# Performance work log

Measured on AMD Instinct MI355X. Metric: run time of the kernel, lower is better.

The kernel has to match this reference:

```python
import jax, jax.numpy as jnp
import numpy as np
from jax import lax

DN = ('NCHW', 'OIHW', 'NCHW')

def conv(x, k):
    return lax.conv_general_dilated(x, k, (1, 1), 'SAME', dimension_numbers=DN)

def conv_adj(y, k):
    # adjoint of SAME stride-1 conv: correlate with spatially-flipped, channel-transposed kernel
    return conv(y, jnp.flip(k, (2, 3)).transpose(1, 0, 2, 3))

def setup_inputs() -> dict:
    key = jax.random.key(0)
    ks = jax.random.split(key, 8)
    B, H, W = 8, 512, 512
    Cw, Ch = 4, 32
    return {
        'sino': jax.random.normal(ks[0], (B, 1, H, W), jnp.float32),
        'x': jax.random.normal(ks[1], (B, 1, H, W), jnp.float32),
        'laam': jnp.asarray([0.05], jnp.float32),
        'miu': jnp.asarray([0.01], jnp.float32),
        'Kw': jax.random.normal(ks[2], (Cw, 1, 3, 3), jnp.float32) * 0.1,
        'Ka': jax.random.normal(ks[3], (1, 1, 5, 5), jnp.float32) * 0.1,
        'W1': jax.random.normal(ks[4], (Ch, 1, 3, 3), jnp.float32) * 0.05,
        'b1': jnp.zeros((Ch,), jnp.float32),
        'W2': jax.random.normal(ks[5], (Ch, Ch, 3, 3), jnp.float32) * 0.05,
        'b2': jnp.zeros((Ch,), jnp.float32),
        'W3': jax.random.normal(ks[6], (1, Ch, 3, 3), jnp.float32) * 0.05,
        'b3': jnp.zeros((1,), jnp.float32),
    }

def reference(sino, x, laam, miu, Kw, Ka, W1, b1, W2, b2, W3, b3):
    mu = miu  # shape (1,), broadcasts as scalar

    def Wop(u):  return conv(u, Kw)          # analysis transform, [B,Cw,H,W]
    def WTop(v): return conv_adj(v, Kw)      # synthesis (adjoint)
    def Aop(u):  return conv(u, Ka)          # system operator surrogate
    def ATop(s): return conv_adj(s, Ka)

    def cnn(u):
        h = jax.nn.relu(conv(u, W1) + b1[None, :, None, None])
        h = jax.nn.relu(conv(h, W2) + b2[None, :, None, None])
        return u + conv(h, W3) + b3[None, :, None, None]

    def AWx(p):  # (A^T A + mu W^T W) p
        return ATop(Aop(p)) + mu * WTop(Wop(p))

    # --- MetaInvH forward ---
    Wu = Wop(x)
    dnz = jax.nn.relu(Wu - laam) - jax.nn.relu(-Wu - laam)  # soft threshold
    rhs = ATop(sino) + WTop(dnz) * miu
    uk0 = cnn(x)
    res = AWx(uk0) - rhs

    # --- CG_alg, 5 iterations + final half step ---
    xk, r, p = uk0, res, -res
    for _ in range(5):
        Ap = Aop(p)                                   # [B,1,H,W]
        Wp = Wop(p)                                   # [B,Cw,H,W]
        pATAp = jnp.sum(Ap * Ap, axis=(1, 2, 3))      # [B]
        pWTWp = mu * jnp.sum(Wp * Wp, axis=(1, 2, 3)) # [B]
        rTr = jnp.sum(r * r, axis=(1, 2, 3))
        al = (rTr / (pWTWp + pATAp))[:, None, None, None]
        xk = xk + al * p
        r = r + al * (ATop(Ap) + mu * WTop(Wp))
        be = (jnp.sum(r * r, axis=(1, 2, 3)) / rTr)[:, None, None, None]
        p = -r + be * p
    Ap = Aop(p)
    Wp = Wop(p)
    pATAp = jnp.sum(Ap * Ap, axis=(1, 2, 3))
    pWTWp = mu * jnp.sum(Wp * Wp, axis=(1, 2, 3))
    rTr = jnp.sum(r * r, axis=(1, 2, 3))
    al = (rTr / (pWTWp + pATAp))[:, None, None, None]
    return xk + al * p
```

## Files before the change

kernel.cpp:

```cpp
#include <hip/hip_runtime.h>

#define HH 512
#define WW 512
#define BB 8
#define IMG (HH*WW)
#define NTOT (BB*IMG)

typedef float f32x4 __attribute__((ext_vector_type(4)));
typedef _Float16 half8 __attribute__((ext_vector_type(8)));

__device__ inline uint f2h2(float a, float b) {
  uint d; asm("v_cvt_pkrtz_f16_f32 %0, %1, %2" : "=v"(d) : "v"(a), "v"(b)); return d;
}
__device__ inline uint pkfma(uint a, uint b, uint c) {
  uint d; asm("v_pk_fma_f16 %0, %1, %2, %3" : "=v"(d) : "v"(a), "v"(b), "v"(c)); return d;
}
__device__ inline uint pkmax0(uint a) {
  uint d, z = 0u; asm("v_pk_max_f16 %0, %1, %2" : "=v"(d) : "v"(a), "v"(z)); return d;
}

__device__ inline void atomic_block_sum(float part, float* red, float* dst) {
  for (int off = 32; off > 0; off >>= 1) part += __shfl_down(part, off, 64);
  int lane = threadIdx.x & 63, w = threadIdx.x >> 6;
  if (lane == 0) red[w] = part;
  __syncthreads();
  if (threadIdx.x == 0) atomicAdd(dst, red[0] + red[1] + red[2] + red[3]);
}

__global__ void k_prep(const float* __restrict__ Ka, const float* __restrict__ Kw,
                       const float* __restrict__ miu,
                       const float* __restrict__ W1, const float* __restrict__ b1,
                       const float* __restrict__ W2, const float* __restrict__ W3,
                       float* __restrict__ G, ushort* __restrict__ w2pk,
                       uint* __restrict__ w1pk, uint* __restrict__ b1pk,
                       ushort* __restrict__ w3fr, float* __restrict__ scal) {
  __shared__ float lka[25], lkw[36], lw1[288], lw3[288];
  int tid = threadIdx.x;
  if (tid < 192) scal[tid] = 0.f;
  if (tid < 25) lka[tid] = Ka[tid];
  if (tid < 36) lkw[tid] = Kw[tid];
  if (tid < 256) { lw1[tid] = W1[tid]; lw3[tid] = W3[tid]; }
  if (tid < 32) { lw1[256+tid] = W1[256+tid]; lw3[256+tid] = W3[256+tid]; }
  __syncthreads();
  if (tid < 81) {
    int oy = tid / 9 - 4, ox = tid % 9 - 4;
    float mu = miu[0];
    float ga = 0.f;
    for (int dy = 0; dy < 5; dy++)
      for (int dx = 0; dx < 5; dx++) {
        int ey = dy + oy, ex = dx + ox;
        if (ey >= 0 && ey < 5 && ex >= 0 && ex < 5) ga += lka[dy*5+dx] * lka[ey*5+ex];
      }
    float gw = 0.f;
    if (oy >= -2 && oy <= 2 && ox >= -2 && ox <= 2) {
      for (int ch = 0; ch < 4; ch++)
        for (int dy = 0; dy < 3; dy++)
          for (int dx = 0; dx < 3; dx++) {
            int ey = dy + oy, ex = dx + ox;
            if (ey >= 0 && ey < 3 && ex >= 0 && ex < 3)
              gw += lkw[ch*9 + dy*3+dx] * lkw[ch*9 + ey*3+ex];
          }
    }
    G[tid] = ga + mu * gw;
  }
  #pragma unroll 1
  for (int k = 0; k < 36; k++) {
    int i = tid + k*256;
    int j = i & 7, l = (i >> 3) & 63, f = i >> 9;
    int t5 = f >> 1, h = f & 1;
    int co = 16*h + (l & 15), ci = 8*(l >> 4) + j;
    w2pk[i] = (ushort)(f2h2(W2[(co*32 + ci)*9 + t5], 0.f) & 0xffffu);
  }
  if (tid < 144) {
    int cp = tid / 9, t = tid % 9;
    w1pk[tid] = f2h2(lw1[(2*cp)*9 + t], lw1[(2*cp+1)*9 + t]);
  }
  if (tid < 16) b1pk[tid] = f2h2(b1[2*tid], b1[2*tid+1]);
  for (int k = 0; k < 2; k++) {
    int i = tid + k*256;
    int j = i & 7, l = i >> 3;
    int tap = l & 15, ch = 8*(l >> 4) + j;
    w3fr[i] = (tap < 9) ? (ushort)(f2h2(lw3[ch*9 + tap], 0.f) & 0xffffu) : (ushort)0;
  }
}

__launch_bounds__(512)
__global__ void k_cnn(const float* __restrict__ x,
                      const ushort* __restrict__ w2pk, const uint* __restrict__ w1pk,
                      const uint* __restrict__ b1pk, const ushort* __restrict__ w3fr,
                      const float* __restrict__ b2, const float* __restrict__ b3,
                      float* __restrict__ xk) {
  __shared__ __align__(16) uint  xs_h2[528];
  __shared__ __align__(16) uint  h1u[7040];
  __shared__ __align__(16) uint  h2u[5472];

  const int tid = threadIdx.x;
  const int bimg = blockIdx.z;
  const int oy0 = blockIdx.y * 16, ox0 = blockIdx.x * 16;
  const float* xim = x + (size_t)bimg * IMG;

  for (int i = tid; i < 528; i += 512) {
    int ly = i / 24, lx = i % 24;
    int gy = oy0 + ly - 3, gx = ox0 + lx - 4;
    float v = 0.f;
    if ((unsigned)gy < HH && (unsigned)gx < WW) v = xim[gy*WW + gx];
    xs_h2[i] = f2h2(v, v);
  }
  __syncthreads();

  {
    const int cp = tid & 15;
    const int sg = tid >> 4;
    uint w1r[9];
    #pragma unroll
    for (int k = 0; k < 9; k++) w1r[k] = w1pk[cp*9 + k];
    const uint b1v = b1pk[cp];
    const int kg = cp >> 2, cl = cp & 3;
    #pragma unroll 1
    for (int s = sg; s < 100; s += 32) {
      int row = s / 5, st = s - 5*row;
      int px0 = st * 4;
      uint acc0 = b1v, acc1 = b1v, acc2 = b1v, acc3 = b1v;
      #pragma unroll
      for (int ky = 0; ky < 3; ky++) {
        int base = (row + ky) * 24 + px0;
        uint4 xa = *(const uint4*)&xs_h2[base];
        uint4 xb = *(const uint4*)&xs_h2[base + 4];
        uint xu[8] = {xa.x, xa.y, xa.z, xa.w, xb.x, xb.y, xb.z, xb.w};
        #pragma unroll
        for (int kx = 0; kx < 3; kx++) {
          uint w = w1r[ky*3 + kx];
          acc0 = pkfma(w, xu[1 + kx], acc0);
          acc1 = pkfma(w, xu[2 + kx], acc1);
          acc2 = pkfma(w, xu[3 + kx], acc2);
          acc3 = pkfma(w, xu[4 + kx], acc3);
        }
      }
      int Y = oy0 + row - 2;
      bool rin = (unsigned)Y < HH;
      int ob = row*352 + kg*88 + px0*4 + cl;
      #pragma unroll
      for (int i = 0; i < 4; i++) {
        int X = ox0 + px0 + i - 2;
        uint v = (rin && (unsigned)X < WW) ?
                 pkmax0(i == 0 ? acc0 : (i == 1 ? acc1 : (i == 2 ? acc2 : acc3))) : 0u;
        h1u[ob + i*4] = v;
      }
    }
  }
  __syncthreads();

  const int wv = tid >> 6, lane = tid & 63;
  const int nn = lane & 15, kg = lane >> 4;
  {
    half8 afr[9][2];
    #pragma unroll
    for (int t5 = 0; t5 < 9; t5++) {
      afr[t5][0] = ((const half8*)w2pk)[(t5*2 + 0)*64 + lane];
      afr[t5][1] = ((const half8*)w2pk)[(t5*2 + 1)*64 + lane];
    }
    float b2A[4], b2B[4];
    #pragma unroll
    for (int j = 0; j < 4; j++) { b2A[j] = b2[4*kg + j]; b2B[j] = b2[16 + 4*kg + j]; }

    #pragma unroll 1
    for (int t = wv; t < 27; t += 8) {
      int rp = t / 3, cs = t - 3*rp;
      int tx0 = (cs == 2) ? 10 : (cs << 3);
      int brow = 2*rp + (nn >> 3);
      int bcol = tx0 + (nn & 7);
      f32x4 accA = {0.f,0.f,0.f,0.f}, accB = {0.f,0.f,0.f,0.f};
      #pragma unroll
      for (int ky = 0; ky < 3; ky++)
        #pragma unroll
        for (int kx = 0; kx < 3; kx++) {
          const half8 bfr = *(const half8*)&h1u[(brow+ky)*352 + kg*88 + (bcol+kx)*4];
          accA = __builtin_amdgcn_mfma_f32_16x16x32_f16(afr[ky*3+kx][0], bfr, accA, 0, 0, 0);
          accB = __builtin_amdgcn_mfma_f32_16x16x32_f16(afr[ky*3+kx][1], bfr, accB, 0, 0, 0);
        }
      int gy = oy0 + brow - 1, gx = ox0 + bcol - 1;
      bool inb = ((unsigned)gy < HH) && ((unsigned)gx < WW);
      float v0 = inb ? fmaxf(accA[0] + b2A[0], 0.f) : 0.f;
      float v1 = inb ? fmaxf(accA[1] + b2A[1], 0.f) : 0.f;
      float v2 = inb ? fmaxf(accA[2] + b2A[2], 0.f) : 0.f;
      float v3 = inb ? fmaxf(accA[3] + b2A[3], 0.f) : 0.f;
      uint2 uA = make_uint2(f2h2(v0, v1), f2h2(v2, v3));
      v0 = inb ? fmaxf(accB[0] + b2B[0], 0.f) : 0.f;
      v1 = inb ? fmaxf(accB[1] + b2B[1], 0.f) : 0.f;
      v2 = inb ? fmaxf(accB[2] + b2B[2], 0.f) : 0.f;
      v3 = inb ? fmaxf(accB[3] + b2B[3], 0.f) : 0.f;
      uint2 uB = make_uint2(f2h2(v0, v1), f2h2(v2, v3));
      int base = brow*304 + bcol*4 + (kg & 1)*2;
      *(uint2*)&h2u[base + (kg >> 1)*76]       = uA;
      *(uint2*)&h2u[base + (2 + (kg >> 1))*76] = uB;
    }
  }
  __syncthreads();

  float* Tlds = (float*)h1u;
  {
    const half8 w3f = ((const half8*)w3fr)[lane];
    const int tap = nn;
    #pragma unroll 1
    for (int t = wv; t < 27; t += 8) {
      int rp = t / 3, cs = t - 3*rp;
      int tx0 = (cs == 2) ? 10 : (cs << 3);
      int ay = 2*rp + (nn >> 3);
      int ax = tx0 + (nn & 7);
      const half8 afrag = *(const half8*)&h2u[ay*304 + kg*76 + ax*4];
      f32x4 z = {0.f,0.f,0.f,0.f};
      f32x4 T4 = __builtin_amdgcn_mfma_f32_16x16x32_f16(afrag, w3f, z, 0, 0, 0);
      if (tap < 9) {
        int ty = 2*rp + (kg >> 1);
        int txb = tx0 + 4*(kg & 1);
        float* dst = &Tlds[ty*180 + tap*20 + txb];
        if (cs == 2) {
          dst[0] = T4[0]; dst[1] = T4[1]; dst[2] = T4[2]; dst[3] = T4[3];
        } else {
          *(f32x4*)dst = T4;
        }
      }
    }
  }
  __syncthreads();

  {
    const int half = tid & 1, px = tid >> 1;
    const int oy = px >> 4, ox = px & 15;
    float s = 0.f;
    if (half == 0) {
      #pragma unroll
      for (int t = 0; t < 4; t++)
        s += Tlds[(oy + t/3)*180 + t*20 + (ox + t%3)];
    } else {
      #pragma unroll
      for (int t = 4; t < 9; t++)
        s += Tlds[(oy + t/3)*180 + t*20 + (ox + t%3)];
    }
    float other = __shfl_xor(s, 1, 64);
    if (half == 0) {
      float tot = s + other + b3[0] + xim[(size_t)(oy0+oy)*WW + ox0 + ox];
      xk[(size_t)bimg*IMG + (size_t)(oy0+oy)*WW + ox0 + ox] = tot;
    }
  }
}

__device__ __forceinline__ void apply_M2(const float (*ssrc)[76], float* bandv,
    const float* Gs, const float* __restrict__ Ka, const float* __restrict__ Kw,
    float mu, int tid, int oy0, int ox0, float* accv) {
  const int sy = tid >> 3, sx0 = (tid & 7) * 8;
  #pragma unroll
  for (int k = 0; k < 8; k++) accv[k] = 0.f;
  #pragma unroll 1
  for (int oyy = 0; oyy < 9; oyy++) {
    float g[9];
    #pragma unroll
    for (int t = 0; t < 9; t++) g[t] = Gs[oyy*9+t];
    const float* row = &ssrc[sy+oyy][sx0];
    float4 r0 = *(const float4*)(row);
    float4 r1 = *(const float4*)(row+4);
    float4 r2 = *(const float4*)(row+8);
    float4 r3 = *(const float4*)(row+12);
    float v[16] = {r0.x,r0.y,r0.z,r0.w, r1.x,r1.y,r1.z,r1.w,
                   r2.x,r2.y,r2.z,r2.w, r3.x,r3.y,r3.z,r3.w};
    #pragma unroll
    for (int k = 0; k < 8; k++) {
      float a = accv[k];
      #pragma unroll
      for (int t = 0; t < 9; t++) a = fmaf(g[t], v[k+t], a);
      accv[k] = a;
    }
  }
  const int by = blockIdx.y, bx = blockIdx.x;
  const bool eT = (by == 0), eB = (by == (int)gridDim.y - 1);
  const bool eL = (bx == 0), eR = (bx == (int)gridDim.x - 1);
  if (eT | eB | eL | eR) {
    const int nTop = eT ? 128 : 0;
    const int nBot = eB ? 128 : 0;
    const int yl = eT ? 2 : 0, yh = eB ? 30 : 32;
    const int nL = eL ? 2*(yh-yl) : 0;
    const int nR = eR ? 2*(yh-yl) : 0;
    const int nBand = nTop + nBot + nL + nR;
    if (tid < nBand) {
      int i = tid, bsy, bsx;
      if (i < nTop) { bsy = i >> 6; bsx = i & 63; }
      else if (i < nTop + nBot) { i -= nTop; bsy = 30 + (i >> 6); bsx = i & 63; }
      else if (i < nTop + nBot + nL) { i -= nTop + nBot; bsy = yl + (i >> 1); bsx = i & 1; }
      else { i -= nTop + nBot + nL; bsy = yl + (i >> 1); bsx = 62 + (i & 1); }
      const int gy = oy0 + bsy, gx = ox0 + bsx;
      float P[9][9];
      #pragma unroll
      for (int r = 0; r < 9; r++)
        #pragma unroll
        for (int c = 0; c < 9; c++) P[r][c] = ssrc[bsy + r][bsx + c];
      float ka[25];
      #pragma unroll
      for (int k = 0; k < 25; k++) ka[k] = Ka[k];
      float qa = 0.f;
      #pragma unroll
      for (int dy = 0; dy < 5; dy++)
        #pragma unroll
        for (int dx = 0; dx < 5; dx++) {
          float inner = 0.f;
          #pragma unroll
          for (int ey = 0; ey < 5; ey++)
            #pragma unroll
            for (int ex = 0; ex < 5; ex++)
              inner = fmaf(ka[ey*5+ex], P[4+ey-dy][4+ex-dx], inner);
          bool ok = ((unsigned)(gy+2-dy) < HH) && ((unsigned)(gx+2-dx) < WW);
          qa = ok ? fmaf(ka[dy*5+dx], inner, qa) : qa;
        }
      float qw = 0.f;
      #pragma unroll
      for (int ch = 0; ch < 4; ch++) {
        float kw[9];
        #pragma unroll
        for (int k = 0; k < 9; k++) kw[k] = Kw[ch*9+k];
        #pragma unroll
        for (int dy = 0; dy < 3; dy++)
          #pragma unroll
          for (int dx = 0; dx < 3; dx++) {
            float inner = 0.f;
            #pragma unroll
            for (int ey = 0; ey < 3; ey++)
              #pragma unroll
              for (int ex = 0; ex < 3; ex++)
                inner = fmaf(kw[ey*3+ex], P[4+ey-dy][4+ex-dx], inner);
            bool ok = ((unsigned)(gy+1-dy) < HH) && ((unsigned)(gx+1-dx) < WW);
            qw = ok ? fmaf(kw[dy*3+dx], inner, qw) : qw;
          }
      }
      bandv[tid] = qa + mu * qw;
    }
    __syncthreads();
    #pragma unroll
    for (int k = 0; k < 8; k++) {
      const int sx = sx0 + k;
      const int gy = oy0 + sy, gx = ox0 + sx;
      if ((gy < 2) || (gy >= HH-2) || (gx < 2) || (gx >= WW-2)) {
        int idx;
        if (eT && sy < 2) idx = sy*64 + sx;
        else if (eB && sy >= 30) idx = nTop + (sy-30)*64 + sx;
        else if (eL && sx < 2) idx = nTop + nBot + (sy-yl)*2 + sx;
        else idx = nTop + nBot + nL + (sy-yl)*2 + (sx-62);
        accv[k] = bandv[idx];
      }
    }
  }
}

__launch_bounds__(256)
__global__ void k_M0(const float* __restrict__ xk, const float* __restrict__ sino,
                     const float* __restrict__ x,
                     float* __restrict__ outR, float* __restrict__ outP,
                     const float* __restrict__ G,
                     const float* __restrict__ Ka, const float* __restrict__ Kw,
                     const float* __restrict__ laam, const float* __restrict__ miu,
                     float* __restrict__ rtrOut) {
  __shared__ __align__(16) float ssrc[40][76];
  __shared__ __align__(16) float tbuf[36][68];
  __shared__ __align__(16) float ssin[36][68];
  __shared__ __align__(16) float sx[36][68];
  __shared__ float Gs[81], kas[25], kws[36];
  __shared__ float red[4];
  const int tid = threadIdx.x;
  const int bimg = blockIdx.z;
  const int oy0 = blockIdx.y*32, ox0 = blockIdx.x*64;
  if (tid < 81) Gs[tid] = G[tid];
  if (tid >= 81 && tid < 106) kas[tid-81] = Ka[tid-81];
  if (tid >= 106 && tid < 142) kws[tid-106] = Kw[tid-106];
  const float mu = miu[0];
  const float lam = laam[0];
  const float* sxk = xk + (size_t)bimg*IMG;
  const float* ssi = sino + (size_t)bimg*IMG;
  const float* sxi = x + (size_t)bimg*IMG;

  for (int i = tid; i < 40*76; i += 256) {
    int ly = i/76, lx = i%76;
    int gy = oy0 + ly - 4, gx = ox0 + lx - 4;
    bool in = (lx < 72) && (gy >= 0 && gy < HH && gx >= 0 && gx < WW);
    ssrc[ly][lx] = in ? sxk[gy*WW+gx] : 0.f;
  }
  for (int i = tid; i < 36*68; i += 256) {
    int ly = i/68, lx = i%68;
    int gy = oy0 + ly - 2, gx = ox0 + lx - 2;
    bool in = (gy >= 0 && gy < HH && gx >= 0 && gx < WW);
    ssin[ly][lx] = in ? ssi[gy*WW+gx] : 0.f;
    sx[ly][lx]   = in ? sxi[gy*WW+gx] : 0.f;
  }
  __syncthreads();

  float accv[8];
  apply_M2(ssrc, &tbuf[0][0], Gs, kas, kws, mu, tid, oy0, ox0, accv);

  const int sy = tid >> 3, sx0 = (tid & 7) * 8;
  float rhsv[8];
  #pragma unroll
  for (int k = 0; k < 8; k++) rhsv[k] = 0.f;
  {
    #pragma unroll
    for (int dy = 0; dy < 5; dy++) {
      const float* row = &ssin[sy+4-dy][sx0];
      float4 r0 = *(const float4*)(row);
      float4 r1 = *(const float4*)(row+4);
      float4 r2 = *(const float4*)(row+8);
      float w[12] = {r0.x,r0.y,r0.z,r0.w, r1.x,r1.y,r1.z,r1.w, r2.x,r2.y,r2.z,r2.w};
      #pragma unroll
      for (int k = 0; k < 8; k++)
        #pragma unroll
        for (int dx = 0; dx < 5; dx++)
          rhsv[k] = fmaf(kas[dy*5+dx], w[k+4-dx], rhsv[k]);
    }
  }
  #pragma unroll 1
  for (int ch = 0; ch < 4; ch++) {
    __syncthreads();
    {
      float kw[9];
      #pragma unroll
      for (int k = 0; k < 9; k++) kw[k] = kws[ch*9 + k];
      #pragma unroll 1
      for (int item = tid; item < 2244; item += 256) {
        int dy = item / 66, dx = item - 66*dy;
        int gy = oy0 + dy - 1, gx = ox0 + dx - 1;
        float v = 0.f;
        if (gy >= 0 && gy < HH && gx >= 0 && gx < WW) {
          float wu = 0.f;
          #pragma unroll
          for (int e = 0; e < 9; e++) wu = fmaf(kw[e], sx[dy + e/3][dx + e%3], wu);
          v = fmaxf(wu - lam, 0.f) - fmaxf(-wu - lam, 0.f);
        }
        tbuf[dy][dx] = v;
      }
    }
    __syncthreads();
    {
      float kw[9];
      #pragma unroll
      for (int k = 0; k < 9; k++) kw[k] = mu * kws[ch*9 + k];
      #pragma unroll
      for (int dy = 0; dy < 3; dy++) {
        const float* row = &tbuf[sy+2-dy][sx0];
        float4 r0 = *(const float4*)(row);
        float4 r1 = *(const float4*)(row+4);
        float4 r2 = *(const float4*)(row+8);
        float w[12] = {r0.x,r0.y,r0.z,r0.w, r1.x,r1.y,r1.z,r1.w, r2.x,r2.y,r2.z,r2.w};
        #pragma unroll
        for (int k = 0; k < 8; k++)
          #pragma unroll
          for (int dx = 0; dx < 3; dx++)
            rhsv[k] = fmaf(kw[dy*3+dx], w[k+2-dx], rhsv[k]);
      }
    }
  }

  const int gy = oy0 + sy, gx0 = ox0 + sx0;
  float part = 0.f;
  #pragma unroll
  for (int k = 0; k < 8; k++) {
    size_t idx = (size_t)bimg*IMG + gy*WW + gx0 + k;
    float rv = accv[k] - rhsv[k];
    outR[idx] = rv;
    outP[idx] = -rv;
    part += rv*rv;
  }
  atomic_block_sum(part, red, &rtrOut[bimg]);
}

template<int MODE>
__launch_bounds__(256)
__global__ void k_M(const float* __restrict__ srcA, const float* __restrict__ srcB,
                    float* __restrict__ outQ, float* __restrict__ outP,
                    const float* __restrict__ G,
                    const float* __restrict__ Ka, const float* __restrict__ Kw,
                    const float* __restrict__ miu,
                    const float* __restrict__ beN, const float* __restrict__ beD,
                    float* __restrict__ acc, float* __restrict__ rqOut,
                    float* __restrict__ qqOut) {
  __shared__ __align__(16) float ssrc[40][76];
  __shared__ float bandv[256];
  __shared__ float Gs[81];
  __shared__ float red[12];
  const int tid = threadIdx.x;
  const int bimg = blockIdx.z;
  const int oy0 = blockIdx.y*32, ox0 = blockIdx.x*64;
  if (tid < 81) Gs[tid] = G[tid];
  const float mu = miu[0];
  float be = 0.f;
  if (MODE == 2) be = beN[bimg] / beD[bimg];
  const float* sA = srcA + (size_t)bimg*IMG;
  const float* sB = (MODE == 2) ? srcB + (size_t)bimg*IMG : nullptr;

  for (int i = tid; i < 40*76; i += 256) {
    int ly = i/76, lx = i%76;
    int gy = oy0 + ly - 4, gx = ox0 + lx - 4;
    bool in = (lx < 72) && (gy >= 0 && gy < HH && gx >= 0 && gx < WW);
    float v = 0.f;
    if (MODE == 2) {
      if (in) {
        v = -sA[gy*WW+gx] + be * sB[gy*WW+gx];
        if (ly >= 4 && ly < 36 && lx >= 4 && lx < 68)
          outP[(size_t)bimg*IMG + gy*WW + gx] = v;
      }
    } else {
      if (in) v = sA[gy*WW+gx];
    }
    ssrc[ly][lx] = v;
  }
  __syncthreads();

  float accv[8];
  apply_M2(ssrc, bandv, Gs, Ka, Kw, mu, tid, oy0, ox0, accv);

  const int sy = tid >> 3, sx0 = (tid & 7) * 8;
  const int gy = oy0 + sy, gx0 = ox0 + sx0;
  if (MODE == 1) {
    float pq = 0.f, qq = 0.f;
    #pragma unroll
    for (int k = 0; k < 8; k++) {
      size_t idx = (size_t)bimg*IMG + gy*WW + gx0 + k;
      float pv = ssrc[sy+4][sx0+4+k];
      float qv = accv[k];
      outQ[idx] = qv;
      pq += pv * qv;
      qq += qv * qv;
    }
    for (int off = 32; off > 0; off >>= 1) {
      pq += __shfl_down(pq, off, 64);
      qq += __shfl_down(qq, off, 64);
    }
    int lane = tid & 63, w = tid >> 6;
    if (lane == 0) { red[w*2] = pq; red[w*2+1] = qq; }
    __syncthreads();
    if (tid == 0) {
      float A = red[0]+red[2]+red[4]+red[6];
      float Q = red[1]+red[3]+red[5]+red[7];
      atomicAdd(&acc[bimg], A);
      if (rqOut) atomicAdd(&rqOut[bimg], -A);
      if (qqOut) atomicAdd(&qqOut[bimg], Q);
    }
  } else {
    float part = 0.f;
    #pragma unroll
    for (int k = 0; k < 8; k++) {
      size_t idx = (size_t)bimg*IMG + gy*WW + gx0 + k;
      float pv = ssrc[sy+4][sx0+4+k];
      outQ[idx] = accv[k];
      part += pv * accv[k];
    }
    atomic_block_sum(part, red, &acc[bimg]);
  }
}

__launch_bounds__(256)
__global__ void k_it(float* __restrict__ xk,
                     const float* __restrict__ rold, float* __restrict__ rnew,
                     const float* __restrict__ pold, float* __restrict__ pnew,
                     const float* __restrict__ qold, float* __restrict__ qnew,
                     const float* __restrict__ G,
                     const float* __restrict__ Ka, const float* __restrict__ Kw,
                     const float* __restrict__ miu,
                     float* __restrict__ scal, int it, int storeQ) {
  __shared__ __align__(16) float ssrc[40][76];
  __shared__ float rlds[2048];
  __shared__ float bandv[256];
  __shared__ float Gs[81];
  __shared__ float red[12];
  const int tid = threadIdx.x;
  const int bimg = blockIdx.z;
  const int oy0 = blockIdx.y*32, ox0 = blockIdx.x*64;
  if (tid < 81) Gs[tid] = G[tid];
  const float mu = miu[0];
  const float den_p = scal[       (it-1)*8 + bimg];
  const float rq_p  = scal[ 48 + (it-1)*8 + bimg];
  const float qq_p  = scal[ 96 + (it-1)*8 + bimg];
  const float rtr_p = scal[144 + (it-1)*8 + bimg];
  const float al = rtr_p / den_p;
  const float rtr_c = fmaf(al, fmaf(al, qq_p, 2.f*rq_p), rtr_p);
  const float be = rtr_c / rtr_p;
  if (tid == 0) scal[144 + it*8 + bimg] = rtr_c;
  const size_t ib = (size_t)bimg*IMG;

  for (int i = tid; i < 40*76; i += 256) {
    int ly = i/76, lx = i%76;
    int gy = oy0 + ly - 4, gx = ox0 + lx - 4;
    bool in = (lx < 72) && (gy >= 0 && gy < HH && gx >= 0 && gx < WW);
    float v = 0.f;
    if (in) {
      size_t g = ib + (size_t)gy*WW + gx;
      float pg = pold[g];
      float rn = fmaf(al, qold[g], rold[g]);
      v = fmaf(be, pg, -rn);
      if (ly >= 4 && ly < 36 && lx >= 4 && lx < 68) {
        pnew[g] = v;
        rnew[g] = rn;
        xk[g] = fmaf(al, pg, xk[g]);
        rlds[(ly-4)*64 + (lx-4)] = rn;
      }
    }
    ssrc[ly][lx] = v;
  }
  __syncthreads();

  float accv[8];
  apply_M2(ssrc, bandv, Gs, Ka, Kw, mu, tid, oy0, ox0, accv);

  const int sy = tid >> 3, sx0 = (tid & 7) * 8;
  const int gy = oy0 + sy, gx0 = ox0 + sx0;
  float s_den = 0.f, s_rq = 0.f, s_qq = 0.f;
  #pragma unroll
  for (int k = 0; k < 8; k++) {
    size_t idx = ib + (size_t)gy*WW + gx0 + k;
    float qv = accv[k];
    float pv = ssrc[sy+4][sx0+4+k];
    float rv = rlds[sy*64 + sx0 + k];
    if (storeQ) qnew[idx] = qv;
    s_den += pv*qv;
    s_rq  += rv*qv;
    s_qq  += qv*qv;
  }
  for (int off = 32; off > 0; off >>= 1) {
    s_den += __shfl_down(s_den, off, 64);
    s_rq  += __shfl_down(s_rq,  off, 64);
    s_qq  += __shfl_down(s_qq,  off, 64);
  }
  int lane = tid & 63, w = tid >> 6;
  if (lane == 0) { red[w*3] = s_den; red[w*3+1] = s_rq; red[w*3+2] = s_qq; }
  __syncthreads();
  if (tid == 0) {
    atomicAdd(&scal[       it*8 + bimg], red[0]+red[3]+red[6]+red[9]);
    atomicAdd(&scal[ 48 + it*8 + bimg], red[1]+red[4]+red[7]+red[10]);
    atomicAdd(&scal[ 96 + it*8 + bimg], red[2]+red[5]+red[8]+red[11]);
  }
}

__launch_bounds__(256)
__global__ void k_upd(float* __restrict__ xk, float* __restrict__ r,
                      const float* __restrict__ p, const float* __restrict__ q,
                      const float* __restrict__ num, const float* __restrict__ den,
                      float* __restrict__ rtrOut) {
  __shared__ float red[4];
  const int tid = threadIdx.x;
  const int bimg = blockIdx.x >> 8;
  const size_t idx4 = (size_t)blockIdx.x * 256 + tid;
  const float al = num[bimg] / den[bimg];
  float4 xv = ((const float4*)xk)[idx4];
  float4 pv = ((const float4*)p)[idx4];
  float4 rv = ((const float4*)r)[idx4];
  float4 qv = ((const float4*)q)[idx4];
  xv.x += al*pv.x; xv.y += al*pv.y; xv.z += al*pv.z; xv.w += al*pv.w;
  rv.x += al*qv.x; rv.y += al*qv.y; rv.z += al*qv.z; rv.w += al*qv.w;
  ((float4*)xk)[idx4] = xv;
  ((float4*)r)[idx4] = rv;
  float part = rv.x*rv.x + rv.y*rv.y + rv.z*rv.z + rv.w*rv.w;
  atomic_block_sum(part, red, &rtrOut[bimg]);
}

__launch_bounds__(256)
__global__ void k_final(const float* __restrict__ xk, const float* __restrict__ p,
                        const float* __restrict__ num, const float* __restrict__ den,
                        float* __restrict__ out) {
  const int tid = threadIdx.x;
  const int bimg = blockIdx.x >> 8;
  const size_t idx4 = (size_t)blockIdx.x * 256 + tid;
  const float al = num[bimg] / den[bimg];
  float4 xv = ((const float4*)xk)[idx4];
  float4 pv = ((const float4*)p)[idx4];
  float4 o;
  o.x = xv.x + al*pv.x; o.y = xv.y + al*pv.y; o.z = xv.z + al*pv.z; o.w = xv.w + al*pv.w;
  ((float4*)out)[idx4] = o;
}

extern "C" void kernel_launch(void* const* d_in, const int* in_sizes, int n_in,
                              void* d_out, int out_size, void* d_ws, size_t ws_size,
                              hipStream_t stream) {
  const float* sino = (const float*)d_in[0];
  const float* x    = (const float*)d_in[1];
  const float* laam = (const float*)d_in[2];
  const float* miu  = (const float*)d_in[3];
  const float* Kw   = (const float*)d_in[4];
  const float* Ka   = (const float*)d_in[5];
  const float* W1   = (const float*)d_in[6];
  const float* b1   = (const float*)d_in[7];
  const float* W2   = (const float*)d_in[8];
  const float* b2   = (const float*)d_in[9];
  const float* W3   = (const float*)d_in[10];
  const float* b3   = (const float*)d_in[11];

  const bool fused = ws_size >= (size_t)6*NTOT*4 + 65536;
  float* ws = (float*)d_ws;
  const size_t nb = fused ? 6 : 5;
  float* tail = ws + nb*(size_t)NTOT;
  float* G    = tail;
  float* scal = tail + 96;
  ushort* w2pk = (ushort*)(scal + 192);
  uint*   w1pk = (uint*)(w2pk + 9216);
  uint*   b1pk = w1pk + 144;
  ushort* w3fr = (ushort*)(b1pk + 16);
  float* dout = (float*)d_out;

  k_prep<<<1, 256, 0, stream>>>(Ka, Kw, miu, W1, b1, W2, W3, G, w2pk, w1pk, b1pk,
                                w3fr, scal);

  float* xk = ws;
  k_cnn<<<dim3(32,32,8), 512, 0, stream>>>(x, w2pk, w1pk, b1pk, w3fr, b2, b3, xk);

  dim3 mg(8,16,8);
  if (fused) {
    float* rA = ws + (size_t)NTOT;
    float* rB = ws + 2*(size_t)NTOT;
    float* pA = ws + 3*(size_t)NTOT;
    float* pB = ws + 4*(size_t)NTOT;
    float* qB = ws + 5*(size_t)NTOT;
    float* qA = dout;
    k_M0<<<mg,256,0,stream>>>(xk, sino, x, rA, pA, G, Ka, Kw, laam, miu, &scal[144]);
    k_M<1><<<mg,256,0,stream>>>(pA, nullptr, qA, nullptr, G, Ka, Kw, miu,
                                nullptr, nullptr, &scal[0], &scal[48], &scal[96]);
    float *rc=rA, *rn=rB, *pc=pA, *pn=pB, *qc=qA, *qn=qB;
    for (int it = 1; it <= 5; it++) {
      k_it<<<mg,256,0,stream>>>(xk, rc, rn, pc, pn, qc, qn, G, Ka, Kw, miu, scal,
                                it, it < 5 ? 1 : 0);
      float* t;
      t = rc; rc = rn; rn = t;
      t = pc; pc = pn; pn = t;
      t = qc; qc = qn; qn = t;
    }
    k_final<<<2048,256,0,stream>>>(xk, pc, &scal[144+40], &scal[40], dout);
  } else {
    float* r  = ws + (size_t)NTOT;
    float* p0 = ws + 2*(size_t)NTOT;
    float* p1 = ws + 3*(size_t)NTOT;
    float* q  = ws + 4*(size_t)NTOT;
    k_M0<<<mg,256,0,stream>>>(xk, sino, x, r, p0, G, Ka, Kw, laam, miu, &scal[144]);
    k_M<1><<<mg,256,0,stream>>>(p0, nullptr, q, nullptr, G, Ka, Kw, miu,
                                nullptr, nullptr, &scal[0], nullptr, nullptr);
    k_upd<<<2048,256,0,stream>>>(xk, r, p0, q, &scal[144], &scal[0], &scal[144+8]);
    float* pcur = p0; float* pnext = p1;
    for (int i = 1; i <= 4; i++) {
      k_M<2><<<mg,256,0,stream>>>(r, pcur, q, pnext, G, Ka, Kw, miu,
                                  &scal[144+8*i], &scal[144+8*(i-1)], &scal[8*i],
                                  nullptr, nullptr);
      k_upd<<<2048,256,0,stream>>>(xk, r, pnext, q, &scal[144+8*i], &scal[8*i],
                                   &scal[144+8*(i+1)]);
      float* t = pcur; pcur = pnext; pnext = t;
    }
    k_M<2><<<mg,256,0,stream>>>(r, pcur, q, pnext, G, Ka, Kw, miu,
                                &scal[144+40], &scal[144+32], &scal[40],
                                nullptr, nullptr);
    k_final<<<2048,256,0,stream>>>(xk, pnext, &scal[144+40], &scal[40], dout);
  }
}
```

Baseline: 388.4 us.

## Precompute per-boundary-class combined stencils for border correction

Replaces the per-thread border correction in apply_M2, which rebuilt the A^T A + mu W^T W operator from the raw Ka/Kw kernels with hundreds of FMAs, with a lookup into 25 precomputed 9x9 stencils, one per edge-position class. The table is built once in k_prep, now launched with 1024 threads, and the interior stencil is taken from the centre entry. k_cnn also aliases its input staging buffer onto h2u to cut shared memory use. The aim is to shorten the edge blocks that stall the CG iteration kernels, at the cost of a larger workspace table and a slightly longer prep kernel.

After: 389.1 us. Within noise of the previous version (+0.2%).

```diff
diff --git a/kernel.cpp b/kernel.cpp
--- a/kernel.cpp
+++ b/kernel.cpp
@@ -27,11 +27,18 @@
   if (threadIdx.x == 0) atomicAdd(dst, red[0] + red[1] + red[2] + red[3]);
 }
 
+__device__ inline bool mA5(int t, int e) {
+  return (t==0) ? (e<=2) : (t==1) ? (e<=3) : (t==3) ? (e>=1) : (t==4) ? (e>=2) : true;
+}
+__device__ inline bool mW3(int t, int e) {
+  return (t==0) ? (e<=1) : (t==4) ? (e>=1) : true;
+}
+
 __global__ void k_prep(const float* __restrict__ Ka, const float* __restrict__ Kw,
                        const float* __restrict__ miu,
                        const float* __restrict__ W1, const float* __restrict__ b1,
                        const float* __restrict__ W2, const float* __restrict__ W3,
-                       float* __restrict__ G, ushort* __restrict__ w2pk,
+                       float* __restrict__ tab, ushort* __restrict__ w2pk,
                        uint* __restrict__ w1pk, uint* __restrict__ b1pk,
                        ushort* __restrict__ w3fr, float* __restrict__ scal) {
   __shared__ float lka[25], lkw[36], lw1[288], lw3[288];
@@ -39,33 +46,37 @@
   if (tid < 192) scal[tid] = 0.f;
   if (tid < 25) lka[tid] = Ka[tid];
   if (tid < 36) lkw[tid] = Kw[tid];
-  if (tid < 256) { lw1[tid] = W1[tid]; lw3[tid] = W3[tid]; }
-  if (tid < 32) { lw1[256+tid] = W1[256+tid]; lw3[256+tid] = W3[256+tid]; }
-  __syncthreads();
-  if (tid < 81) {
-    int oy = tid / 9 - 4, ox = tid % 9 - 4;
-    float mu = miu[0];
-    float ga = 0.f;
-    for (int dy = 0; dy < 5; dy++)
-      for (int dx = 0; dx < 5; dx++) {
-        int ey = dy + oy, ex = dx + ox;
-        if (ey >= 0 && ey < 5 && ex >= 0 && ex < 5) ga += lka[dy*5+dx] * lka[ey*5+ex];
-      }
-    float gw = 0.f;
-    if (oy >= -2 && oy <= 2 && ox >= -2 && ox <= 2) {
+  if (tid < 288) { lw1[tid] = W1[tid]; lw3[tid] = W3[tid]; }
+  __syncthreads();
+  const float mu = miu[0];
+  #pragma unroll
+  for (int k = 0; k < 2; k++) {
+    int idx = tid + k*1024;
+    if (idx < 2025) {
+      int c = idx / 81, o = idx - c*81;
+      int ty = c / 5, tx = c - 5*ty;
+      int uy = o / 9 - 4, ux = o % 9 - 4;
+      float s = 0.f;
+      for (int ey = 0; ey < 5; ey++)
+        for (int ex = 0; ex < 5; ex++) {
+          int dy = ey + uy, dx = ex + ux;
+          if (dy >= 0 && dy < 5 && dx >= 0 && dx < 5 && mA5(ty,ey) && mA5(tx,ex))
+            s += lka[ey*5+ex] * lka[dy*5+dx];
+        }
+      float sw = 0.f;
       for (int ch = 0; ch < 4; ch++)
-        for (int dy = 0; dy < 3; dy++)
-          for (int dx = 0; dx < 3; dx++) {
-            int ey = dy + oy, ex = dx + ox;
-            if (ey >= 0 && ey < 3 && ex >= 0 && ex < 3)
-              gw += lkw[ch*9 + dy*3+dx] * lkw[ch*9 + ey*3+ex];
+        for (int ey = 0; ey < 3; ey++)
+          for (int ex = 0; ex < 3; ex++) {
+            int dy = ey + uy, dx = ex + ux;
+            if (dy >= 0 && dy < 3 && dx >= 0 && dx < 3 && mW3(ty,ey) && mW3(tx,ex))
+              sw += lkw[ch*9+ey*3+ex] * lkw[ch*9+dy*3+dx];
           }
-    }
-    G[tid] = ga + mu * gw;
-  }
-  #pragma unroll 1
-  for (int k = 0; k < 36; k++) {
-    int i = tid + k*256;
+      tab[idx] = s + mu * sw;
+    }
+  }
+  #pragma unroll
+  for (int k = 0; k < 9; k++) {
+    int i = tid + k*1024;
     int j = i & 7, l = (i >> 3) & 63, f = i >> 9;
     int t5 = f >> 1, h = f & 1;
     int co = 16*h + (l & 15), ci = 8*(l >> 4) + j;
@@ -76,11 +87,10 @@
     w1pk[tid] = f2h2(lw1[(2*cp)*9 + t], lw1[(2*cp+1)*9 + t]);
   }
   if (tid < 16) b1pk[tid] = f2h2(b1[2*tid], b1[2*tid+1]);
-  for (int k = 0; k < 2; k++) {
-    int i = tid + k*256;
-    int j = i & 7, l = i >> 3;
+  if (tid < 512) {
+    int j = tid & 7, l = tid >> 3;
     int tap = l & 15, ch = 8*(l >> 4) + j;
-    w3fr[i] = (tap < 9) ? (ushort)(f2h2(lw3[ch*9 + tap], 0.f) & 0xffffu) : (ushort)0;
+    w3fr[tid] = (tap < 9) ? (ushort)(f2h2(lw3[ch*9 + tap], 0.f) & 0xffffu) : (ushort)0;
   }
 }
 
@@ -90,9 +100,9 @@
                       const uint* __restrict__ b1pk, const ushort* __restrict__ w3fr,
                       const float* __restrict__ b2, const float* __restrict__ b3,
                       float* __restrict__ xk) {
-  __shared__ __align__(16) uint  xs_h2[528];
   __shared__ __align__(16) uint  h1u[7040];
   __shared__ __align__(16) uint  h2u[5472];
+  uint* xs_h2 = h2u;
 
   const int tid = threadIdx.x;
   const int bimg = blockIdx.z;
@@ -246,8 +256,8 @@
 }
 
 __device__ __forceinline__ void apply_M2(const float (*ssrc)[76], float* bandv,
-    const float* Gs, const float* __restrict__ Ka, const float* __restrict__ Kw,
-    float mu, int tid, int oy0, int ox0, float* accv) {
+    const float* Gs, const float* __restrict__ tab,
+    int tid, int oy0, int ox0, float* accv) {
   const int sy = tid >> 3, sx0 = (tid & 7) * 8;
   #pragma unroll
   for (int k = 0; k < 8; k++) accv[k] = 0.f;
@@ -288,49 +298,21 @@
       else if (i < nTop + nBot + nL) { i -= nTop + nBot; bsy = yl + (i >> 1); bsx = i & 1; }
       else { i -= nTop + nBot + nL; bsy = yl + (i >> 1); bsx = 62 + (i & 1); }
       const int gy = oy0 + bsy, gx = ox0 + bsx;
-      float P[9][9];
-      #pragma unroll
-      for (int r = 0; r < 9; r++)
-        #pragma unroll
-        for (int c = 0; c < 9; c++) P[r][c] = ssrc[bsy + r][bsx + c];
-      float ka[25];
-      #pragma unroll
-      for (int k = 0; k < 25; k++) ka[k] = Ka[k];
-      float qa = 0.f;
-      #pragma unroll
-      for (int dy = 0; dy < 5; dy++)
-        #pragma unroll
-        for (int dx = 0; dx < 5; dx++) {
-          float inner = 0.f;
-          #pragma unroll
-          for (int ey = 0; ey < 5; ey++)
-            #pragma unroll
-            for (int ex = 0; ex < 5; ex++)
-              inner = fmaf(ka[ey*5+ex], P[4+ey-dy][4+ex-dx], inner);
-          bool ok = ((unsigned)(gy+2-dy) < HH) && ((unsigned)(gx+2-dx) < WW);
-          qa = ok ? fmaf(ka[dy*5+dx], inner, qa) : qa;
-        }
-      float qw = 0.f;
-      #pragma unroll
-      for (int ch = 0; ch < 4; ch++) {
-        float kw[9];
-        #pragma unroll
-        for (int k = 0; k < 9; k++) kw[k] = Kw[ch*9+k];
-        #pragma unroll
-        for (int dy = 0; dy < 3; dy++)
-          #pragma unroll
-          for (int dx = 0; dx < 3; dx++) {
-            float inner = 0.f;
-            #pragma unroll
-            for (int ey = 0; ey < 3; ey++)
-              #pragma unroll
-              for (int ex = 0; ex < 3; ex++)
-                inner = fmaf(kw[ey*3+ex], P[4+ey-dy][4+ex-dx], inner);
-            bool ok = ((unsigned)(gy+1-dy) < HH) && ((unsigned)(gx+1-dx) < WW);
-            qw = ok ? fmaf(kw[dy*3+dx], inner, qw) : qw;
-          }
-      }
-      bandv[tid] = qa + mu * qw;
+      int ty = (gy == 0) ? 0 : (gy == 1) ? 1 : (gy == HH-1) ? 4 : (gy == HH-2) ? 3 : 2;
+      int tx = (gx == 0) ? 0 : (gx == 1) ? 1 : (gx == WW-1) ? 4 : (gx == WW-2) ? 3 : 2;
+      const float* S = tab + (ty*5 + tx)*81;
+      float a = 0.f;
+      #pragma unroll
+      for (int oy = 0; oy < 9; oy++) {
+        float s0 = S[oy*9+0], s1 = S[oy*9+1], s2 = S[oy*9+2];
+        float s3 = S[oy*9+3], s4 = S[oy*9+4], s5 = S[oy*9+5];
+        float s6 = S[oy*9+6], s7 = S[oy*9+7], s8 = S[oy*9+8];
+        const float* r = &ssrc[bsy+oy][bsx];
+        a = fmaf(s0, r[0], a); a = fmaf(s1, r[1], a); a = fmaf(s2, r[2], a);
+        a = fmaf(s3, r[3], a); a = fmaf(s4, r[4], a); a = fmaf(s5, r[5], a);
+        a = fmaf(s6, r[6], a); a = fmaf(s7, r[7], a); a = fmaf(s8, r[8], a);
+      }
+      bandv[tid] = a;
     }
     __syncthreads();
     #pragma unroll
@@ -353,7 +335,7 @@
 __global__ void k_M0(const float* __restrict__ xk, const float* __restrict__ sino,
                      const float* __restrict__ x,
                      float* __restrict__ outR, float* __restrict__ outP,
-                     const float* __restrict__ G,
+                     const float* __restrict__ tab,
                      const float* __restrict__ Ka, const float* __restrict__ Kw,
                      const float* __restrict__ laam, const float* __restrict__ miu,
                      float* __restrict__ rtrOut) {
@@ -366,7 +348,7 @@
   const int tid = threadIdx.x;
   const int bimg = blockIdx.z;
   const int oy0 = blockIdx.y*32, ox0 = blockIdx.x*64;
-  if (tid < 81) Gs[tid] = G[tid];
+  if (tid < 81) Gs[tid] = tab[972 + tid];
   if (tid >= 81 && tid < 106) kas[tid-81] = Ka[tid-81];
   if (tid >= 106 && tid < 142) kws[tid-106] = Kw[tid-106];
   const float mu = miu[0];
@@ -391,7 +373,7 @@
   __syncthreads();
 
   float accv[8];
-  apply_M2(ssrc, &tbuf[0][0], Gs, kas, kws, mu, tid, oy0, ox0, accv);
+  apply_M2(ssrc, &tbuf[0][0], Gs, tab, tid, oy0, ox0, accv);
 
   const int sy = tid >> 3, sx0 = (tid & 7) * 8;
   float rhsv[8];
@@ -471,8 +453,7 @@
 __launch_bounds__(256)
 __global__ void k_M(const float* __restrict__ srcA, const float* __restrict__ srcB,
                     float* __restrict__ outQ, float* __restrict__ outP,
-                    const float* __restrict__ G,
-                    const float* __restrict__ Ka, const float* __restrict__ Kw,
+                    const float* __restrict__ tab,
                     const float* __restrict__ miu,
                     const float* __restrict__ beN, const float* __restrict__ beD,
                     float* __restrict__ acc, float* __restrict__ rqOut,
@@ -484,8 +465,7 @@
   const int tid = threadIdx.x;
   const int bimg = blockIdx.z;
   const int oy0 = blockIdx.y*32, ox0 = blockIdx.x*64;
-  if (tid < 81) Gs[tid] = G[tid];
-  const float mu = miu[0];
+  if (tid < 81) Gs[tid] = tab[972 + tid];
   float be = 0.f;
   if (MODE == 2) be = beN[bimg] / beD[bimg];
   const float* sA = srcA + (size_t)bimg*IMG;
@@ -510,7 +490,7 @@
   __syncthreads();
 
   float accv[8];
-  apply_M2(ssrc, bandv, Gs, Ka, Kw, mu, tid, oy0, ox0, accv);
+  apply_M2(ssrc, bandv, Gs, tab, tid, oy0, ox0, accv);
 
   const int sy = tid >> 3, sx0 = (tid & 7) * 8;
   const int gy = oy0 + sy, gx0 = ox0 + sx0;
@@ -557,9 +537,7 @@
                      const float* __restrict__ rold, float* __restrict__ rnew,
                      const float* __restrict__ pold, float* __restrict__ pnew,
                      const float* __restrict__ qold, float* __restrict__ qnew,
-                     const float* __restrict__ G,
-                     const float* __restrict__ Ka, const float* __restrict__ Kw,
-                     const float* __restrict__ miu,
+                     const float* __restrict__ tab,
                      float* __restrict__ scal, int it, int storeQ) {
   __shared__ __align__(16) float ssrc[40][76];
   __shared__ float rlds[2048];
@@ -569,8 +547,7 @@
   const int tid = threadIdx.x;
   const int bimg = blockIdx.z;
   const int oy0 = blockIdx.y*32, ox0 = blockIdx.x*64;
-  if (tid < 81) Gs[tid] = G[tid];
-  const float mu = miu[0];
+  if (tid < 81) Gs[tid] = tab[972 + tid];
   const float den_p = scal[       (it-1)*8 + bimg];
   const float rq_p  = scal[ 48 + (it-1)*8 + bimg];
   const float qq_p  = scal[ 96 + (it-1)*8 + bimg];
@@ -603,7 +580,7 @@
   __syncthreads();
 
   float accv[8];
-  apply_M2(ssrc, bandv, Gs, Ka, Kw, mu, tid, oy0, ox0, accv);
+  apply_M2(ssrc, bandv, Gs, tab, tid, oy0, ox0, accv);
 
   const int sy = tid >> 3, sx0 = (tid & 7) * 8;
   const int gy = oy0 + sy, gx0 = ox0 + sx0;
@@ -691,16 +668,16 @@
   float* ws = (float*)d_ws;
   const size_t nb = fused ? 6 : 5;
   float* tail = ws + nb*(size_t)NTOT;
-  float* G    = tail;
-  float* scal = tail + 96;
+  float* tab  = tail;
+  float* scal = tail + 2048;
   ushort* w2pk = (ushort*)(scal + 192);
   uint*   w1pk = (uint*)(w2pk + 9216);
   uint*   b1pk = w1pk + 144;
   ushort* w3fr = (ushort*)(b1pk + 16);
   float* dout = (float*)d_out;
 
-  k_prep<<<1, 256, 0, stream>>>(Ka, Kw, miu, W1, b1, W2, W3, G, w2pk, w1pk, b1pk,
-                                w3fr, scal);
+  k_prep<<<1, 1024, 0, stream>>>(Ka, Kw, miu, W1, b1, W2, W3, tab, w2pk, w1pk,
+                                 b1pk, w3fr, scal);
 
   float* xk = ws;
   k_cnn<<<dim3(32,32,8), 512, 0, stream>>>(x, w2pk, w1pk, b1pk, w3fr, b2, b3, xk);
@@ -713,12 +690,12 @@
     float* pB = ws + 4*(size_t)NTOT;
     float* qB = ws + 5*(size_t)NTOT;
     float* qA = dout;
-    k_M0<<<mg,256,0,stream>>>(xk, sino, x, rA, pA, G, Ka, Kw, laam, miu, &scal[144]);
-    k_M<1><<<mg,256,0,stream>>>(pA, nullptr, qA, nullptr, G, Ka, Kw, miu,
+    k_M0<<<mg,256,0,stream>>>(xk, sino, x, rA, pA, tab, Ka, Kw, laam, miu, &scal[144]);
+    k_M<1><<<mg,256,0,stream>>>(pA, nullptr, qA, nullptr, tab, miu,
                                 nullptr, nullptr, &scal[0], &scal[48], &scal[96]);
     float *rc=rA, *rn=rB, *pc=pA, *pn=pB, *qc=qA, *qn=qB;
     for (int it = 1; it <= 5; it++) {
-      k_it<<<mg,256,0,stream>>>(xk, rc, rn, pc, pn, qc, qn, G, Ka, Kw, miu, scal,
+      k_it<<<mg,256,0,stream>>>(xk, rc, rn, pc, pn, qc, qn, tab, scal,
                                 it, it < 5 ? 1 : 0);
       float* t;
       t = rc; rc = rn; rn = t;
@@ -731,20 +708,20 @@
     float* p0 = ws + 2*(size_t)NTOT;
     float* p1 = ws + 3*(size_t)NTOT;
     float* q  = ws + 4*(size_t)NTOT;
-    k_M0<<<mg,256,0,stream>>>(xk, sino, x, r, p0, G, Ka, Kw, laam, miu, &scal[144]);
-    k_M<1><<<mg,256,0,stream>>>(p0, nullptr, q, nullptr, G, Ka, Kw, miu,
+    k_M0<<<mg,256,0,stream>>>(xk, sino, x, r, p0, tab, Ka, Kw, laam, miu, &scal[144]);
+    k_M<1><<<mg,256,0,stream>>>(p0, nullptr, q, nullptr, tab, miu,
                                 nullptr, nullptr, &scal[0], nullptr, nullptr);
     k_upd<<<2048,256,0,stream>>>(xk, r, p0, q, &scal[144], &scal[0], &scal[144+8]);
     float* pcur = p0; float* pnext = p1;
     for (int i = 1; i <= 4; i++) {
-      k_M<2><<<mg,256,0,stream>>>(r, pcur, q, pnext, G, Ka, Kw, miu,
+      k_M<2><<<mg,256,0,stream>>>(r, pcur, q, pnext, tab, miu,
                                   &scal[144+8*i], &scal[144+8*(i-1)], &scal[8*i],
                                   nullptr, nullptr);
       k_upd<<<2048,256,0,stream>>>(xk, r, pnext, q, &scal[144+8*i], &scal[8*i],
                                    &scal[144+8*(i+1)]);
       float* t = pcur; pcur = pnext; pnext = t;
     }
-    k_M<2><<<mg,256,0,stream>>>(r, pcur, q, pnext, G, Ka, Kw, miu,
+    k_M<2><<<mg,256,0,stream>>>(r, pcur, q, pnext, tab, miu,
                                 &scal[144+40], &scal[144+32], &scal[40],
                                 nullptr, nullptr);
     k_final<<<2048,256,0,stream>>>(xk, pnext, &scal[144+40], &scal[40], dout);
```
